# Optimization experiments

Measured on AMD Instinct MI355X. Metric: run time of the kernel, lower is better.

## Reference

```python
import jax, jax.numpy as jnp
import numpy as np

N_USER = 100000
N_ITEM = 50000
N = N_USER + N_ITEM          # total graph nodes
D = 64                        # embed_size
NNZ = 4_000_000               # nonzeros in normalized adjacency
LAYERS = 3
B = 2048                      # batch_size
NEG = 4 * B                   # 4 negatives per positive (see create_bpr_loss)


def setup_inputs() -> dict:
    key = jax.random.key(0)
    ks = jax.random.split(key, 8)
    user_emb = jax.random.normal(ks[0], (N_USER, D), dtype=jnp.float32) * 0.1
    item_emb = jax.random.normal(ks[1], (N_ITEM, D), dtype=jnp.float32) * 0.1
    adj_row = jax.random.randint(ks[2], (NNZ,), 0, N, dtype=jnp.int32)
    adj_col = jax.random.randint(ks[3], (NNZ,), 0, N, dtype=jnp.int32)
    # symmetric-normalized adjacency values are small positive floats
    adj_val = jax.random.uniform(ks[4], (NNZ,), dtype=jnp.float32) * 0.05
    users = jax.random.randint(ks[5], (B,), 0, N_USER, dtype=jnp.int32)
    pos_items = jax.random.randint(ks[6], (B,), 0, N_ITEM, dtype=jnp.int32)
    neg_items = jax.random.randint(ks[7], (NEG,), 0, N_ITEM, dtype=jnp.int32)
    mask = jnp.zeros((1,), dtype=jnp.float32)      # unused in mode='plain'
    norm_adj = jnp.zeros((1,), dtype=jnp.float32)  # unused when attention=False
    return {
        "users": users, "pos_items": pos_items, "neg_items": neg_items,
        "mask": mask, "norm_adj": norm_adj,
        "user_emb": user_emb, "item_emb": item_emb,
        "adj_row": adj_row, "adj_col": adj_col, "adj_val": adj_val,
    }


def _spmm(row, col, val, x):
    """Sparse [N,N] @ dense [N,D] via gather + segment_sum."""
    gathered = val[:, None] * x[col]                      # [NNZ, D]
    return jax.ops.segment_sum(gathered, row, num_segments=N)


def reference(users, pos_items, neg_items, mask, norm_adj,
              user_emb, item_emb, adj_row, adj_col, adj_val):
    # ego embeddings for all nodes
    e0 = jnp.concatenate([user_emb, item_emb], axis=0)    # [N, D]
    # NOTE: the original torch code never updates ego_embeddings inside the
    # layer loop, so every layer appends the SAME A_hat @ E0. Hence:
    # light_out = mean([E0, A@E0, A@E0, ..., A@E0]) = (E0 + L*A@E0)/(L+1)
    ae0 = _spmm(adj_row, adj_col, adj_val, e0)            # [N, D]
    light_out = (e0 + LAYERS * ae0) / (LAYERS + 1)
    u_g = light_out[:N_USER]
    i_g = light_out[N_USER:]
    u_g_embeddings = u_g[users]
    pos_i_g_embeddings = i_g[pos_items]
    neg_i_g_embeddings = i_g[neg_items]
    return (u_g_embeddings, pos_i_g_embeddings, neg_i_g_embeddings)
```

## Files before the change

### kernel.cpp

```cpp
#include <hip/hip_runtime.h>

#define N_USER 100000
#define N_ITEM 50000
#define NTOT   150000
#define D      64
#define NNZ    4000000
#define NQ     (NNZ / 4)
#define B      2048
#define NEG    8192
#define NSLOT  (B + B + NEG)
#define CAP    128
#define NBW    ((NTOT + 31) / 32)

__device__ __forceinline__ int slot_row(int slot,
                                        const int* __restrict__ users,
                                        const int* __restrict__ pos,
                                        const int* __restrict__ neg) {
    if (slot < B)     return users[slot];
    if (slot < 2 * B) return N_USER + pos[slot - B];
    return N_USER + neg[slot - 2 * B];
}

__device__ __forceinline__ const float* e0_row(int c,
                                               const float* __restrict__ ue,
                                               const float* __restrict__ ie) {
    return (c < N_USER) ? &ue[(size_t)c * D] : &ie[(size_t)(c - N_USER) * D];
}

__global__ void k_clear(unsigned int* __restrict__ bits) {
    int i = blockIdx.x * blockDim.x + threadIdx.x;
    if (i < NBW) bits[i] = 0u;
}

__global__ void k_mark(const int* __restrict__ users,
                       const int* __restrict__ pos,
                       const int* __restrict__ neg,
                       unsigned int* __restrict__ bits,
                       int* __restrict__ rowslot,
                       int* __restrict__ cnt,
                       float* __restrict__ accd) {
    int slot = (blockIdx.x * blockDim.x + threadIdx.x) >> 6;
    int lane = threadIdx.x & 63;
    if (slot >= NSLOT) return;
    int r = slot_row(slot, users, pos, neg);
    int won = 0;
    if (lane == 0) {
        unsigned int bit = 1u << (r & 31);
        unsigned int old = atomicOr(&bits[r >> 5], bit);
        won = (old & bit) ? 0 : 1;
        if (won) { rowslot[r] = slot; cnt[slot] = 0; }
    }
    won = __shfl(won, 0);
    if (won) accd[(size_t)slot * D + lane] = 0.0f;
}

__global__ __launch_bounds__(1024)
void k_scan(const int*   __restrict__ adj_row,
            const int*   __restrict__ adj_col,
            const float* __restrict__ adj_val,
            const float* __restrict__ ue,
            const float* __restrict__ ie,
            const unsigned int* __restrict__ bits,
            const int*   __restrict__ rowslot,
            int*   __restrict__ cnt,
            int2*  __restrict__ bcv,
            float* __restrict__ accd) {
    __shared__ unsigned int sbits[NBW];
    {
        const int4* gb = (const int4*)bits;
        int4* sb = (int4*)sbits;
        for (int i = threadIdx.x; i < NBW / 4; i += blockDim.x) sb[i] = gb[i];
    }
    __syncthreads();

    int tid = blockIdx.x * blockDim.x + threadIdx.x;
    int nth = gridDim.x * blockDim.x;
    const int4*   row4 = (const int4*)adj_row;
    const int4*   col4 = (const int4*)adj_col;
    const float4* val4 = (const float4*)adj_val;

    #define PROC(RR, CC, VV)                                               \
    {                                                                      \
        unsigned int w = sbits[(RR) >> 5];                                 \
        if ((w >> ((RR) & 31)) & 1u) {                                     \
            int s = rowslot[RR];                                           \
            int idx = atomicAdd(&cnt[s], 1);                               \
            if (idx < CAP) {                                               \
                bcv[(size_t)s * CAP + idx] = make_int2(CC, __float_as_int(VV)); \
            } else {       \
                const float* x = e0_row(CC, ue, ie);                       \
                for (int d = 0; d < D; ++d)                                \
                    atomicAdd(&accd[(size_t)s * D + d], (VV) * x[d]);      \
            }                                                              \
        }                                                                  \
    }

    int g = tid;
    if (g >= NQ) return;
    int4   r = row4[g];
    int4   c = col4[g];
    float4 v = val4[g];
    for (;;) {
        int gn = g + nth;
        bool more = gn < NQ;
        int4 rn, cn; float4 vn;
        if (more) { rn = row4[gn]; cn = col4[gn]; vn = val4[gn]; }
        PROC(r.x, c.x, v.x)
        PROC(r.y, c.y, v.y)
        PROC(r.z, c.z, v.z)
        PROC(r.w, c.w, v.w)
        if (!more) break;
        g = gn; r = rn; c = cn; v = vn;
    }
    #undef PROC
}

__global__ void k_rowacc(const int* __restrict__ users,
                         const int* __restrict__ pos,
                         const int* __restrict__ neg,
                         const int* __restrict__ rowslot,
                         const int* __restrict__ cnt,
                         const int2* __restrict__ bcv,
                         const float* __restrict__ ue,
                         const float* __restrict__ ie,
                         float* __restrict__ accd) {
    int slot = (blockIdx.x * blockDim.x + threadIdx.x) >> 6;
    int lane = threadIdx.x & 63;
    if (slot >= NSLOT) return;
    int r = slot_row(slot, users, pos, neg);
    if (rowslot[r] != slot) return;
    int n = cnt[slot];
    if (n > CAP) n = CAP;
    const int2* bb = &bcv[(size_t)slot * CAP];
    int sub = lane & 15, grp = lane >> 4;
    float4 a = make_float4(0.f, 0.f, 0.f, 0.f);
    for (int i = 0; i < n; i += 16) {
        int m  = n - 1;
        int e0 = i + grp, e1 = e0 + 4, e2 = e0 + 8, e3 = e0 + 12;
        int2 p0 = bb[min(e0, m)];
        int2 p1 = bb[min(e1, m)];
        int2 p2 = bb[min(e2, m)];
        int2 p3 = bb[min(e3, m)];
        float4 x0 = ((const float4*)e0_row(p0.x, ue, ie))[sub];
        float4 x1 = ((const float4*)e0_row(p1.x, ue, ie))[sub];
        float4 x2 = ((const float4*)e0_row(p2.x, ue, ie))[sub];
        float4 x3 = ((const float4*)e0_row(p3.x, ue, ie))[sub];
        float v0 = (e0 < n) ? __int_as_float(p0.y) : 0.f;
        float v1 = (e1 < n) ? __int_as_float(p1.y) : 0.f;
        float v2 = (e2 < n) ? __int_as_float(p2.y) : 0.f;
        float v3 = (e3 < n) ? __int_as_float(p3.y) : 0.f;
        a.x += v0 * x0.x; a.y += v0 * x0.y; a.z += v0 * x0.z; a.w += v0 * x0.w;
        a.x += v1 * x1.x; a.y += v1 * x1.y; a.z += v1 * x1.z; a.w += v1 * x1.w;
        a.x += v2 * x2.x; a.y += v2 * x2.y; a.z += v2 * x2.z; a.w += v2 * x2.w;
        a.x += v3 * x3.x; a.y += v3 * x3.y; a.z += v3 * x3.z; a.w += v3 * x3.w;
    }
    a.x += __shfl_xor(a.x, 16); a.y += __shfl_xor(a.y, 16);
    a.z += __shfl_xor(a.z, 16); a.w += __shfl_xor(a.w, 16);
    a.x += __shfl_xor(a.x, 32); a.y += __shfl_xor(a.y, 32);
    a.z += __shfl_xor(a.z, 32); a.w += __shfl_xor(a.w, 32);
    if (grp == 0) {
        float4* dst = (float4*)&accd[(size_t)slot * D];
        float4 o = dst[sub];
        dst[sub] = make_float4(o.x + a.x, o.y + a.y, o.z + a.z, o.w + a.w);
    }
}

__global__ void k_out(const int* __restrict__ users,
                      const int* __restrict__ pos,
                      const int* __restrict__ neg,
                      const float* __restrict__ ue,
                      const float* __restrict__ ie,
                      const int* __restrict__ rowslot,
                      const float* __restrict__ accd,
                      float* __restrict__ out) {
    int slot = (blockIdx.x * blockDim.x + threadIdx.x) >> 6;
    int lane = threadIdx.x & 63;
    if (slot >= NSLOT) return;
    int r = slot_row(slot, users, pos, neg);
    float e = (r < N_USER) ? ue[(size_t)r * D + lane]
                           : ie[(size_t)(r - N_USER) * D + lane];
    int id = rowslot[r];
    out[(size_t)slot * D + lane] = 0.25f * e + 0.75f * accd[(size_t)id * D + lane];
}

extern "C" void kernel_launch(void* const* d_in, const int* in_sizes, int n_in,
                              void* d_out, int out_size, void* d_ws, size_t ws_size,
                              hipStream_t stream) {
    const int*   users   = (const int*)  d_in[0];
    const int*   pos     = (const int*)  d_in[1];
    const int*   neg     = (const int*)  d_in[2];
    const float* ue      = (const float*)d_in[5];
    const float* ie      = (const float*)d_in[6];
    const int*   adj_row = (const int*)  d_in[7];
    const int*   adj_col = (const int*)  d_in[8];
    const float* adj_val = (const float*)d_in[9];
    float*       out     = (float*)      d_out;

    char* w = (char*)d_ws;
    int*          rowslot = (int*)w;          w += (size_t)NTOT * sizeof(int);
    unsigned int* bits    = (unsigned int*)w; w += (size_t)NBW * sizeof(unsigned int);
    int*          cnt     = (int*)w;          w += (size_t)NSLOT * sizeof(int);
    int2*         bcv     = (int2*)w;         w += (size_t)NSLOT * CAP * sizeof(int2);
    float*        accd    = (float*)w;

    k_clear <<<(NBW + 255) / 256, 256, 0, stream>>>(bits);
    k_mark  <<<(NSLOT * 64 + 255) / 256, 256, 0, stream>>>(users, pos, neg,
                                                           bits, rowslot, cnt, accd);
    k_scan  <<<256, 1024, 0, stream>>>(adj_row, adj_col, adj_val, ue, ie,
                                       bits, rowslot, cnt, bcv, accd);
    k_rowacc<<<(NSLOT * 64 + 255) / 256, 256, 0, stream>>>(users, pos, neg,
                                                           rowslot, cnt, bcv,
                                                           ue, ie, accd);
    k_out   <<<(NSLOT * 64 + 255) / 256, 256, 0, stream>>>(users, pos, neg, ue, ie,
                                                           rowslot, accd, out);
}
```

Before: 163.2 us.

## Fuse row accumulation with output, drop dense accumulator, rescan on overflow

Merges the per-row accumulation and output kernels into a single finishing kernel that accumulates in registers and writes the blended result directly. This removes the accd buffer, its zeroing in the mark kernel, and the slow atomic fallback for rows over capacity. Overflowing rows, expected to be rare, instead rescan the whole adjacency list inside the finishing kernel. The mark kernel becomes one thread per slot, and the scan launch changes from 256x1024 to 1024x512 threads. The rescan path costs a full 4M-entry pass per overflowing row, so it would be very slow if any row exceeded the capacity.

After: 158.8 us. 2.7% less time.

```diff
diff --git a/kernel.cpp b/kernel.cpp
--- a/kernel.cpp
+++ b/kernel.cpp
@@ -37,34 +37,26 @@
                        const int* __restrict__ neg,
                        unsigned int* __restrict__ bits,
                        int* __restrict__ rowslot,
-                       int* __restrict__ cnt,
-                       float* __restrict__ accd) {
-    int slot = (blockIdx.x * blockDim.x + threadIdx.x) >> 6;
-    int lane = threadIdx.x & 63;
+                       int* __restrict__ cnt) {
+    int slot = blockIdx.x * blockDim.x + threadIdx.x;
     if (slot >= NSLOT) return;
     int r = slot_row(slot, users, pos, neg);
-    int won = 0;
-    if (lane == 0) {
-        unsigned int bit = 1u << (r & 31);
-        unsigned int old = atomicOr(&bits[r >> 5], bit);
-        won = (old & bit) ? 0 : 1;
-        if (won) { rowslot[r] = slot; cnt[slot] = 0; }
-    }
-    won = __shfl(won, 0);
-    if (won) accd[(size_t)slot * D + lane] = 0.0f;
-}
-
-__global__ __launch_bounds__(1024)
+    unsigned int bit = 1u << (r & 31);
+    unsigned int old = atomicOr(&bits[r >> 5], bit);
+    if (!(old & bit)) {
+        rowslot[r] = slot;
+        cnt[slot]  = 0;
+    }
+}
+
+__global__ __launch_bounds__(512)
 void k_scan(const int*   __restrict__ adj_row,
             const int*   __restrict__ adj_col,
             const float* __restrict__ adj_val,
-            const float* __restrict__ ue,
-            const float* __restrict__ ie,
             const unsigned int* __restrict__ bits,
             const int*   __restrict__ rowslot,
             int*   __restrict__ cnt,
-            int2*  __restrict__ bcv,
-            float* __restrict__ accd) {
+            int2*  __restrict__ bcv) {
     __shared__ unsigned int sbits[NBW];
     {
         const int4* gb = (const int4*)bits;
@@ -79,20 +71,15 @@
     const int4*   col4 = (const int4*)adj_col;
     const float4* val4 = (const float4*)adj_val;
 
-    #define PROC(RR, CC, VV)                                               \
-    {                                                                      \
-        unsigned int w = sbits[(RR) >> 5];                                 \
-        if ((w >> ((RR) & 31)) & 1u) {                                     \
-            int s = rowslot[RR];                                           \
-            int idx = atomicAdd(&cnt[s], 1);                               \
-            if (idx < CAP) {                                               \
+    #define PROC(RR, CC, VV)                                                    \
+    {                                                                           \
+        unsigned int w = sbits[(RR) >> 5];                                      \
+        if ((w >> ((RR) & 31)) & 1u) {                                          \
+            int s = rowslot[RR];                                                \
+            int idx = atomicAdd(&cnt[s], 1);                                    \
+            if (idx < CAP)                                                      \
                 bcv[(size_t)s * CAP + idx] = make_int2(CC, __float_as_int(VV)); \
-            } else {       \
-                const float* x = e0_row(CC, ue, ie);                       \
-                for (int d = 0; d < D; ++d)                                \
-                    atomicAdd(&accd[(size_t)s * D + d], (VV) * x[d]);      \
-            }                                                              \
-        }                                                                  \
+        }                                                                       \
     }
 
     int g = tid;
@@ -115,72 +102,72 @@
     #undef PROC
 }
 
-__global__ void k_rowacc(const int* __restrict__ users,
-                         const int* __restrict__ pos,
-                         const int* __restrict__ neg,
-                         const int* __restrict__ rowslot,
-                         const int* __restrict__ cnt,
-                         const int2* __restrict__ bcv,
-                         const float* __restrict__ ue,
-                         const float* __restrict__ ie,
-                         float* __restrict__ accd) {
-    int slot = (blockIdx.x * blockDim.x + threadIdx.x) >> 6;
-    int lane = threadIdx.x & 63;
-    if (slot >= NSLOT) return;
-    int r = slot_row(slot, users, pos, neg);
-    if (rowslot[r] != slot) return;
-    int n = cnt[slot];
-    if (n > CAP) n = CAP;
-    const int2* bb = &bcv[(size_t)slot * CAP];
-    int sub = lane & 15, grp = lane >> 4;
-    float4 a = make_float4(0.f, 0.f, 0.f, 0.f);
-    for (int i = 0; i < n; i += 16) {
-        int m  = n - 1;
-        int e0 = i + grp, e1 = e0 + 4, e2 = e0 + 8, e3 = e0 + 12;
-        int2 p0 = bb[min(e0, m)];
-        int2 p1 = bb[min(e1, m)];
-        int2 p2 = bb[min(e2, m)];
-        int2 p3 = bb[min(e3, m)];
-        float4 x0 = ((const float4*)e0_row(p0.x, ue, ie))[sub];
-        float4 x1 = ((const float4*)e0_row(p1.x, ue, ie))[sub];
-        float4 x2 = ((const float4*)e0_row(p2.x, ue, ie))[sub];
-        float4 x3 = ((const float4*)e0_row(p3.x, ue, ie))[sub];
-        float v0 = (e0 < n) ? __int_as_float(p0.y) : 0.f;
-        float v1 = (e1 < n) ? __int_as_float(p1.y) : 0.f;
-        float v2 = (e2 < n) ? __int_as_float(p2.y) : 0.f;
-        float v3 = (e3 < n) ? __int_as_float(p3.y) : 0.f;
-        a.x += v0 * x0.x; a.y += v0 * x0.y; a.z += v0 * x0.z; a.w += v0 * x0.w;
-        a.x += v1 * x1.x; a.y += v1 * x1.y; a.z += v1 * x1.z; a.w += v1 * x1.w;
-        a.x += v2 * x2.x; a.y += v2 * x2.y; a.z += v2 * x2.z; a.w += v2 * x2.w;
-        a.x += v3 * x3.x; a.y += v3 * x3.y; a.z += v3 * x3.z; a.w += v3 * x3.w;
-    }
-    a.x += __shfl_xor(a.x, 16); a.y += __shfl_xor(a.y, 16);
-    a.z += __shfl_xor(a.z, 16); a.w += __shfl_xor(a.w, 16);
-    a.x += __shfl_xor(a.x, 32); a.y += __shfl_xor(a.y, 32);
-    a.z += __shfl_xor(a.z, 32); a.w += __shfl_xor(a.w, 32);
-    if (grp == 0) {
-        float4* dst = (float4*)&accd[(size_t)slot * D];
-        float4 o = dst[sub];
-        dst[sub] = make_float4(o.x + a.x, o.y + a.y, o.z + a.z, o.w + a.w);
-    }
-}
-
-__global__ void k_out(const int* __restrict__ users,
+__global__ void k_fin(const int* __restrict__ users,
                       const int* __restrict__ pos,
                       const int* __restrict__ neg,
+                      const int* __restrict__ rowslot,
+                      const int* __restrict__ cnt,
+                      const int2* __restrict__ bcv,
+                      const int*   __restrict__ adj_row,
+                      const int*   __restrict__ adj_col,
+                      const float* __restrict__ adj_val,
                       const float* __restrict__ ue,
                       const float* __restrict__ ie,
-                      const int* __restrict__ rowslot,
-                      const float* __restrict__ accd,
                       float* __restrict__ out) {
     int slot = (blockIdx.x * blockDim.x + threadIdx.x) >> 6;
     int lane = threadIdx.x & 63;
     if (slot >= NSLOT) return;
     int r = slot_row(slot, users, pos, neg);
-    float e = (r < N_USER) ? ue[(size_t)r * D + lane]
-                           : ie[(size_t)(r - N_USER) * D + lane];
-    int id = rowslot[r];
-    out[(size_t)slot * D + lane] = 0.25f * e + 0.75f * accd[(size_t)id * D + lane];
+    int owner = rowslot[r];
+    int n = cnt[owner];
+    int sub = lane & 15, grp = lane >> 4;
+    float4 a = make_float4(0.f, 0.f, 0.f, 0.f);
+
+    if (n <= CAP) {
+        const int2* bb = &bcv[(size_t)owner * CAP];
+        for (int i = 0; i < n; i += 16) {
+            int m  = n - 1;
+            int e0 = i + grp, e1 = e0 + 4, e2 = e0 + 8, e3 = e0 + 12;
+            int2 p0 = bb[min(e0, m)];
+            int2 p1 = bb[min(e1, m)];
+            int2 p2 = bb[min(e2, m)];
+            int2 p3 = bb[min(e3, m)];
+            float4 x0 = ((const float4*)e0_row(p0.x, ue, ie))[sub];
+            float4 x1 = ((const float4*)e0_row(p1.x, ue, ie))[sub];
+            float4 x2 = ((const float4*)e0_row(p2.x, ue, ie))[sub];
+            float4 x3 = ((const float4*)e0_row(p3.x, ue, ie))[sub];
+            float v0 = (e0 < n) ? __int_as_float(p0.y) : 0.f;
+            float v1 = (e1 < n) ? __int_as_float(p1.y) : 0.f;
+            float v2 = (e2 < n) ? __int_as_float(p2.y) : 0.f;
+            float v3 = (e3 < n) ? __int_as_float(p3.y) : 0.f;
+            a.x += v0 * x0.x; a.y += v0 * x0.y; a.z += v0 * x0.z; a.w += v0 * x0.w;
+            a.x += v1 * x1.x; a.y += v1 * x1.y; a.z += v1 * x1.z; a.w += v1 * x1.w;
+            a.x += v2 * x2.x; a.y += v2 * x2.y; a.z += v2 * x2.z; a.w += v2 * x2.w;
+            a.x += v3 * x3.x; a.y += v3 * x3.y; a.z += v3 * x3.z; a.w += v3 * x3.w;
+        }
+    } else {
+        for (int e = grp; e < NNZ; e += 4) {
+            if (adj_row[e] == r) {
+                float v = adj_val[e];
+                float4 x = ((const float4*)e0_row(adj_col[e], ue, ie))[sub];
+                a.x += v * x.x; a.y += v * x.y; a.z += v * x.z; a.w += v * x.w;
+            }
+        }
+    }
+
+    a.x += __shfl_xor(a.x, 16); a.y += __shfl_xor(a.y, 16);
+    a.z += __shfl_xor(a.z, 16); a.w += __shfl_xor(a.w, 16);
+    a.x += __shfl_xor(a.x, 32); a.y += __shfl_xor(a.y, 32);
+    a.z += __shfl_xor(a.z, 32); a.w += __shfl_xor(a.w, 32);
+
+    if (grp == 0) {
+        float4 e = ((const float4*)e0_row(r, ue, ie))[sub];
+        float4* o = (float4*)&out[(size_t)slot * D];
+        o[sub] = make_float4(0.25f * e.x + 0.75f * a.x,
+                             0.25f * e.y + 0.75f * a.y,
+                             0.25f * e.z + 0.75f * a.z,
+                             0.25f * e.w + 0.75f * a.w);
+    }
 }
 
 extern "C" void kernel_launch(void* const* d_in, const int* in_sizes, int n_in,
@@ -200,17 +187,15 @@
     int*          rowslot = (int*)w;          w += (size_t)NTOT * sizeof(int);
     unsigned int* bits    = (unsigned int*)w; w += (size_t)NBW * sizeof(unsigned int);
     int*          cnt     = (int*)w;          w += (size_t)NSLOT * sizeof(int);
-    int2*         bcv     = (int2*)w;         w += (size_t)NSLOT * CAP * sizeof(int2);
-    float*        accd    = (float*)w;
-
-    k_clear <<<(NBW + 255) / 256, 256, 0, stream>>>(bits);
-    k_mark  <<<(NSLOT * 64 + 255) / 256, 256, 0, stream>>>(users, pos, neg,
-                                                           bits, rowslot, cnt, accd);
-    k_scan  <<<256, 1024, 0, stream>>>(adj_row, adj_col, adj_val, ue, ie,
-                                       bits, rowslot, cnt, bcv, accd);
-    k_rowacc<<<(NSLOT * 64 + 255) / 256, 256, 0, stream>>>(users, pos, neg,
-                                                           rowslot, cnt, bcv,
-                                                           ue, ie, accd);
-    k_out   <<<(NSLOT * 64 + 255) / 256, 256, 0, stream>>>(users, pos, neg, ue, ie,
-                                                           rowslot, accd, out);
-}
+    int2*         bcv     = (int2*)w;
+
+    k_clear<<<(NBW + 255) / 256, 256, 0, stream>>>(bits);
+    k_mark <<<(NSLOT + 255) / 256, 256, 0, stream>>>(users, pos, neg,
+                                                     bits, rowslot, cnt);
+    k_scan <<<1024, 512, 0, stream>>>(adj_row, adj_col, adj_val,
+                                      bits, rowslot, cnt, bcv);
+    k_fin  <<<(NSLOT * 64 + 255) / 256, 256, 0, stream>>>(users, pos, neg,
+                                                          rowslot, cnt, bcv,
+                                                          adj_row, adj_col, adj_val,
+                                                          ue, ie, out);
+}
```
